# Optimization experiments

Hardware: AMD Instinct MI355X
Metric: run time of the kernel (lower is better)

## Reference

```python
import jax, jax.numpy as jnp
import numpy as np

N_HEAD = 12

def setup_inputs() -> dict:
    key = jax.random.key(0)
    k1, k2, k3 = jax.random.split(key, 3)
    B, T, C = 8, 1024, 768
    x = jax.random.normal(k1, (B, T, C), dtype=jnp.float32)
    # Linear weights stored as [in, out] so y = x @ W + b (same math as torch Linear)
    w_attn = jax.random.normal(k2, (C, 3 * C), dtype=jnp.float32) * (1.0 / np.sqrt(C))
    b_attn = jnp.zeros((3 * C,), dtype=jnp.float32)
    w_proj = jax.random.normal(k3, (C, C), dtype=jnp.float32) * (1.0 / np.sqrt(C))
    b_proj = jnp.zeros((C,), dtype=jnp.float32)
    return {"x": x, "w_attn": w_attn, "b_attn": b_attn, "w_proj": w_proj, "b_proj": b_proj}

def reference(x, w_attn, b_attn, w_proj, b_proj):
    B, T, C = x.shape
    H = N_HEAD
    D = C // H
    qkv = x @ w_attn + b_attn                        # [B,T,3C]
    q, k, v = jnp.split(qkv, 3, axis=-1)             # each [B,T,C]
    q = q.reshape(B, T, H, D).transpose(0, 2, 1, 3)  # [B,H,T,D]
    k = k.reshape(B, T, H, D).transpose(0, 2, 1, 3)
    v = v.reshape(B, T, H, D).transpose(0, 2, 1, 3)
    scale = 1.0 / jnp.sqrt(jnp.asarray(D, dtype=x.dtype))
    att = jnp.einsum('bhqd,bhkd->bhqk', q, k) * scale  # [B,H,T,T]
    causal = jnp.tril(jnp.ones((T, T), dtype=bool))    # [T,T]
    att = jnp.where(causal[None, None], att, jnp.asarray(-jnp.inf, dtype=att.dtype))
    att = jax.nn.softmax(att, axis=-1)
    out = jnp.einsum('bhqk,bhkd->bhqd', att, v)        # [B,H,T,D]
    out = out.transpose(0, 2, 1, 3).reshape(B, T, C)
    return out @ w_proj + b_proj
```

## Files before the change

### kernel.cpp

```cpp
#include <hip/hip_runtime.h>
#include <hip/hip_bf16.h>
#include <cmath>

#define B_ 8
#define T_ 1024
#define C_ 768
#define H_ 12
#define D_ 64
#define N3C 2304
#define M_ 8192

typedef __bf16 bf16x8 __attribute__((ext_vector_type(8)));
typedef float  f32x4  __attribute__((ext_vector_type(4)));

typedef const __attribute__((address_space(1))) void* gptr_t;
typedef __attribute__((address_space(3))) void* lptr_t;

__device__ __forceinline__ bf16x8 cvt_bf16x8(const float4& a, const float4& b) {
    bf16x8 r;
    r[0] = (__bf16)a.x; r[1] = (__bf16)a.y; r[2] = (__bf16)a.z; r[3] = (__bf16)a.w;
    r[4] = (__bf16)b.x; r[5] = (__bf16)b.y; r[6] = (__bf16)b.z; r[7] = (__bf16)b.w;
    return r;
}

__global__ __launch_bounds__(256) void cast_bf16_k(const float* __restrict__ in,
                                                   __bf16* __restrict__ out, int n) {
    int i = (blockIdx.x * 256 + threadIdx.x) * 8;
    if (i >= n) return;
    float4 a = *(const float4*)&in[i];
    float4 b = *(const float4*)&in[i + 4];
    bf16x8 r = cvt_bf16x8(a, b);
    *(bf16x8*)&out[i] = r;
}

__global__ __launch_bounds__(256) void transpose_cast_k(const float* __restrict__ w,
                                                        __bf16* __restrict__ wt,
                                                        int K, int N) {
    __shared__ float tile[32][33];
    int tx = threadIdx.x, ty = threadIdx.y;
    int n0 = blockIdx.x * 32, k0 = blockIdx.y * 32;
#pragma unroll
    for (int i = 0; i < 4; i++)
        tile[ty + i * 8][tx] = w[(size_t)(k0 + ty + i * 8) * N + n0 + tx];
    __syncthreads();
#pragma unroll
    for (int i = 0; i < 4; i++)
        wt[(size_t)(n0 + ty + i * 8) * K + k0 + tx] = (__bf16)tile[tx][ty + i * 8];
}

__global__ __launch_bounds__(256) void qkv_gemm_mfma(const __bf16* __restrict__ A,
                                                     const __bf16* __restrict__ Bt,
                                                     const float* __restrict__ bias,
                                                     __bf16* __restrict__ qb,
                                                     __bf16* __restrict__ kb,
                                                     __bf16* __restrict__ vbt) {
    __shared__ __bf16 smem[128 * 136];
    __bf16* As = smem;
    __bf16* Bs = smem + 128 * 64;
    const int tid = threadIdx.x;
    const int wave = tid >> 6, lane = tid & 63;
    const int lane15 = lane & 15, quad = lane >> 4;
    const int m0 = blockIdx.y * 128, n0 = blockIdx.x * 128;
    const int wm = (wave >> 1) * 64, wn = (wave & 1) * 64;
    f32x4 acc[4][4] = {};

    for (int k0 = 0; k0 < 768; k0 += 64) {
#pragma unroll
        for (int r = 0; r < 4; ++r) {
            int p = r * 256 + tid;
            int mrow = p >> 3, csw = p & 7;
            int ksrc = (csw ^ (mrow & 7)) * 8;
            __builtin_amdgcn_global_load_lds(
                (gptr_t)(A + (size_t)(m0 + mrow) * 768 + k0 + ksrc),
                (lptr_t)(As + (r * 256 + wave * 64) * 8), 16, 0, 0);
            __builtin_amdgcn_global_load_lds(
                (gptr_t)(Bt + (size_t)(n0 + mrow) * 768 + k0 + ksrc),
                (lptr_t)(Bs + (r * 256 + wave * 64) * 8), 16, 0, 0);
        }
        __syncthreads();
#pragma unroll
        for (int ks = 0; ks < 2; ++ks) {
            bf16x8 af[4], bf[4];
#pragma unroll
            for (int mt = 0; mt < 4; ++mt) {
                int m = wm + mt * 16 + lane15;
                int csw = (ks * 4 + quad) ^ (m & 7);
                af[mt] = *(const bf16x8*)(As + m * 64 + csw * 8);
            }
#pragma unroll
            for (int nt = 0; nt < 4; ++nt) {
                int n = wn + nt * 16 + lane15;
                int csw = (ks * 4 + quad) ^ (n & 7);
                bf[nt] = *(const bf16x8*)(Bs + n * 64 + csw * 8);
            }
#pragma unroll
            for (int mt = 0; mt < 4; ++mt)
#pragma unroll
                for (int nt = 0; nt < 4; ++nt)
                    acc[mt][nt] = __builtin_amdgcn_mfma_f32_16x16x32_bf16(af[mt], bf[nt], acc[mt][nt], 0, 0, 0);
        }
        __syncthreads();
    }

    if (n0 < 1536) {
        const bool isq = (n0 < 768);
        const float sc = isq ? 0.125f : 1.0f;
#pragma unroll
        for (int nt = 0; nt < 4; ++nt) {
            int n = n0 + wn + nt * 16 + lane15;
            int rem = isq ? n : (n - 768);
            int h = rem >> 6;
            int d = n & 63;
            float bv = bias[n];
            __bf16* dst = isq ? qb : kb;
#pragma unroll
            for (int mt = 0; mt < 4; ++mt) {
#pragma unroll
                for (int reg = 0; reg < 4; ++reg) {
                    int mrow = m0 + wm + mt * 16 + quad * 4 + reg;
                    int bb = mrow >> 10, t = mrow & 1023;
                    dst[(((size_t)bb * H_ + h) * T_ + t) * D_ + d] =
                        (__bf16)((acc[mt][nt][reg] + bv) * sc);
                }
            }
        }
    } else {
        __bf16* vls = smem;
#pragma unroll
        for (int nt = 0; nt < 4; ++nt) {
            int nl = wn + nt * 16 + lane15;
            float bv = bias[n0 + nl];
#pragma unroll
            for (int mt = 0; mt < 4; ++mt)
#pragma unroll
                for (int reg = 0; reg < 4; ++reg)
                    vls[nl * 136 + wm + mt * 16 + quad * 4 + reg] =
                        (__bf16)(acc[mt][nt][reg] + bv);
        }
        __syncthreads();
        int nl = tid >> 1;
        int t0 = (tid & 1) * 64;
        int n = n0 + nl;
        int h = (n - 1536) >> 6;
        int d = n & 63;
        int bb = m0 >> 10, tg = (m0 & 1023) + t0;
        __bf16* dst = vbt + (((size_t)bb * H_ + h) * D_ + d) * T_ + tg;
        const __bf16* srcl = vls + nl * 136 + t0;
#pragma unroll
        for (int c = 0; c < 8; ++c)
            *(bf16x8*)(dst + c * 8) = *(const bf16x8*)(srcl + c * 8);
    }
}

__global__ __launch_bounds__(256) void proj_gemm_mfma(const __bf16* __restrict__ A,
                                                      const __bf16* __restrict__ Bt,
                                                      const float* __restrict__ bias,
                                                      float* __restrict__ out) {
    __shared__ __bf16 As[128 * 64];
    __shared__ __bf16 Bs[64 * 64];
    const int tid = threadIdx.x;
    const int wave = tid >> 6, lane = tid & 63;
    const int lane15 = lane & 15, quad = lane >> 4;
    const int m0 = blockIdx.y * 128, n0 = blockIdx.x * 64;
    const int wm = wave * 32;
    f32x4 acc[2][4] = {};

    for (int k0 = 0; k0 < 768; k0 += 64) {
#pragma unroll
        for (int r = 0; r < 4; ++r) {
            int p = r * 256 + tid;
            int mrow = p >> 3, csw = p & 7;
            int ksrc = (csw ^ (mrow & 7)) * 8;
            __builtin_amdgcn_global_load_lds(
                (gptr_t)(A + (size_t)(m0 + mrow) * 768 + k0 + ksrc),
                (lptr_t)(As + (r * 256 + wave * 64) * 8), 16, 0, 0);
        }
#pragma unroll
        for (int r = 0; r < 2; ++r) {
            int p = r * 256 + tid;
            int nrow = p >> 3, csw = p & 7;
            int ksrc = (csw ^ (nrow & 7)) * 8;
            __builtin_amdgcn_global_load_lds(
                (gptr_t)(Bt + (size_t)(n0 + nrow) * 768 + k0 + ksrc),
                (lptr_t)(Bs + (r * 256 + wave * 64) * 8), 16, 0, 0);
        }
        __syncthreads();
#pragma unroll
        for (int ks = 0; ks < 2; ++ks) {
            bf16x8 af[2], bf[4];
#pragma unroll
            for (int mt = 0; mt < 2; ++mt) {
                int m = wm + mt * 16 + lane15;
                int csw = (ks * 4 + quad) ^ (m & 7);
                af[mt] = *(const bf16x8*)(As + m * 64 + csw * 8);
            }
#pragma unroll
            for (int nt = 0; nt < 4; ++nt) {
                int n = nt * 16 + lane15;
                int csw = (ks * 4 + quad) ^ (n & 7);
                bf[nt] = *(const bf16x8*)(Bs + n * 64 + csw * 8);
            }
#pragma unroll
            for (int mt = 0; mt < 2; ++mt)
#pragma unroll
                for (int nt = 0; nt < 4; ++nt)
                    acc[mt][nt] = __builtin_amdgcn_mfma_f32_16x16x32_bf16(af[mt], bf[nt], acc[mt][nt], 0, 0, 0);
        }
        __syncthreads();
    }

#pragma unroll
    for (int nt = 0; nt < 4; ++nt) {
        int n = n0 + nt * 16 + lane15;
        float bv = bias[n];
#pragma unroll
        for (int mt = 0; mt < 2; ++mt) {
#pragma unroll
            for (int reg = 0; reg < 4; ++reg) {
                int mrow = m0 + wm + mt * 16 + quad * 4 + reg;
                out[(size_t)mrow * C_ + n] = acc[mt][nt][reg] + bv;
            }
        }
    }
}

__global__ __launch_bounds__(256) void attn_mfma(const __bf16* __restrict__ qb,
                                                 const __bf16* __restrict__ kb,
                                                 const __bf16* __restrict__ vbt,
                                                 __bf16* __restrict__ ao) {
    __shared__ __bf16 Ks[64 * 64];
    __shared__ __bf16 Vts[64 * 64];
    __shared__ __bf16 Ps[4 * 32 * 72];

    const int tid = threadIdx.x;
    const int wave = tid >> 6, lane = tid & 63;
    const int lane15 = lane & 15, quad = lane >> 4;
    const int bh = blockIdx.x;
    const int qt = 7 - blockIdx.y;
    const int b = bh / H_, h = bh % H_;
    const int q0 = qt * 128;

    const __bf16* Kb = kb + (size_t)bh * T_ * D_;
    const __bf16* Vb = vbt + (size_t)bh * D_ * T_;
    __bf16* Pw = Ps + wave * 32 * 72;

    bf16x8 qf[2][2];
#pragma unroll
    for (int g = 0; g < 2; ++g) {
        const __bf16* qrow = qb + ((size_t)bh * T_ + q0 + wave * 32 + g * 16 + lane15) * D_ + quad * 8;
        qf[g][0] = *(const bf16x8*)qrow;
        qf[g][1] = *(const bf16x8*)(qrow + 32);
    }

    f32x4 o[2][4] = {};
    float lsum[2][4] = {};

    const int kunits = 2 * qt + 2;
    for (int ku = 0; ku < kunits; ++ku) {
        const int k0 = ku * 64;
#pragma unroll
        for (int r = 0; r < 2; ++r) {
            int p = r * 256 + tid;
            int row = p >> 3, c = p & 7;
            int cs = (c ^ (row & 7)) * 8;
            __builtin_amdgcn_global_load_lds(
                (gptr_t)(Kb + (size_t)(k0 + row) * D_ + cs),
                (lptr_t)(Ks + (r * 256 + wave * 64) * 8), 16, 0, 0);
            __builtin_amdgcn_global_load_lds(
                (gptr_t)(Vb + (size_t)row * T_ + k0 + cs),
                (lptr_t)(Vts + (r * 256 + wave * 64) * 8), 16, 0, 0);
        }
        __syncthreads();

        f32x4 s[2][4];
#pragma unroll
        for (int kt = 0; kt < 4; ++kt) {
            int row = kt * 16 + lane15;
            bf16x8 kf0 = *(const bf16x8*)(Ks + row * 64 + ((quad) ^ (row & 7)) * 8);
            bf16x8 kf1 = *(const bf16x8*)(Ks + row * 64 + ((4 + quad) ^ (row & 7)) * 8);
#pragma unroll
            for (int g = 0; g < 2; ++g) {
                f32x4 t = {};
                t = __builtin_amdgcn_mfma_f32_16x16x32_bf16(qf[g][0], kf0, t, 0, 0, 0);
                t = __builtin_amdgcn_mfma_f32_16x16x32_bf16(qf[g][1], kf1, t, 0, 0, 0);
                s[g][kt] = t;
            }
        }

        const bool diag = (ku >= 2 * qt);
#pragma unroll
        for (int g = 0; g < 2; ++g) {
#pragma unroll
            for (int kt = 0; kt < 4; ++kt) {
                int col = k0 + kt * 16 + lane15;
#pragma unroll
                for (int r = 0; r < 4; ++r) {
                    float p = __expf(s[g][kt][r]);
                    if (diag) {
                        int qrow = q0 + wave * 32 + g * 16 + quad * 4 + r;
                        if (col > qrow) p = 0.f;
                    }
                    lsum[g][r] += p;
                    Pw[(g * 16 + quad * 4 + r) * 72 + kt * 16 + lane15] = (__bf16)p;
                }
            }
        }

        bf16x8 vf[4][2];
#pragma unroll
        for (int dt = 0; dt < 4; ++dt) {
            int row = dt * 16 + lane15;
#pragma unroll
            for (int half = 0; half < 2; ++half)
                vf[dt][half] = *(const bf16x8*)(Vts + row * 64 + ((half * 4 + quad) ^ (row & 7)) * 8);
        }
#pragma unroll
        for (int g = 0; g < 2; ++g) {
#pragma unroll
            for (int half = 0; half < 2; ++half) {
                bf16x8 pf = *(const bf16x8*)(Pw + (g * 16 + lane15) * 72 + half * 32 + quad * 8);
#pragma unroll
                for (int dt = 0; dt < 4; ++dt)
                    o[g][dt] = __builtin_amdgcn_mfma_f32_16x16x32_bf16(pf, vf[dt][half], o[g][dt], 0, 0, 0);
            }
        }
        __syncthreads();
    }

#pragma unroll
    for (int g = 0; g < 2; ++g) {
        float inv[4];
#pragma unroll
        for (int r = 0; r < 4; ++r) {
            float ls = lsum[g][r];
            ls += __shfl_xor(ls, 1);
            ls += __shfl_xor(ls, 2);
            ls += __shfl_xor(ls, 4);
            ls += __shfl_xor(ls, 8);
            inv[r] = 1.0f / ls;
        }
#pragma unroll
        for (int dt = 0; dt < 4; ++dt) {
#pragma unroll
            for (int r = 0; r < 4; ++r) {
                int t = q0 + wave * 32 + g * 16 + quad * 4 + r;
                ao[((size_t)(b * T_ + t)) * C_ + h * 64 + dt * 16 + lane15] =
                    (__bf16)(o[g][dt][r] * inv[r]);
            }
        }
    }
}

extern "C" void kernel_launch(void* const* d_in, const int* in_sizes, int n_in,
                              void* d_out, int out_size, void* d_ws, size_t ws_size,
                              hipStream_t stream) {
    const float* x = (const float*)d_in[0];
    const float* w_attn = (const float*)d_in[1];
    const float* b_attn = (const float*)d_in[2];
    const float* w_proj = (const float*)d_in[3];
    const float* b_proj = (const float*)d_in[4];
    float* out = (float*)d_out;

    __bf16* xb = (__bf16*)d_ws;
    __bf16* wat = xb + (size_t)M_ * C_;
    __bf16* wpt = wat + (size_t)N3C * C_;
    __bf16* qb = wpt + (size_t)C_ * C_;
    __bf16* kb = qb + (size_t)96 * T_ * D_;
    __bf16* vbt = kb + (size_t)96 * T_ * D_;
    __bf16* ao = vbt + (size_t)96 * T_ * D_;

    cast_bf16_k<<<(M_ * C_) / (256 * 8), 256, 0, stream>>>(x, xb, M_ * C_);
    transpose_cast_k<<<dim3(N3C / 32, C_ / 32), dim3(32, 8), 0, stream>>>(w_attn, wat, C_, N3C);
    transpose_cast_k<<<dim3(C_ / 32, C_ / 32), dim3(32, 8), 0, stream>>>(w_proj, wpt, C_, C_);

    qkv_gemm_mfma<<<dim3(N3C / 128, M_ / 128), 256, 0, stream>>>(xb, wat, b_attn, qb, kb, vbt);
    attn_mfma<<<dim3(96, 8), 256, 0, stream>>>(qb, kb, vbt, ao);
    proj_gemm_mfma<<<dim3(C_ / 64, M_ / 128), 256, 0, stream>>>(ao, wpt, b_proj, out);
}
```

Measured before the change: 199.7 us.

## Double-buffer attention K/V tiles, use exp2 softmax, fuse prepass casts

The attention kernel now double-buffers its K and V tiles in LDS. The next tile's global_load_lds is issued before computing on the current tile, and one barrier per iteration is dropped. Q is pre-scaled by log2(e) in the QKV epilogue so the softmax can use the hardware exp2 instruction instead of __expf. The three prepass kernels (x cast and two weight transpose-casts) are merged into a single launch to cut launch overhead. The cost is doubled LDS for K and V, which may reduce occupancy, and correctness now depends on the earlier barrier protecting the buffer being overwritten.

```diff
diff --git a/kernel.cpp b/kernel.cpp
--- a/kernel.cpp
+++ b/kernel.cpp
@@ -16,6 +16,8 @@
 typedef const __attribute__((address_space(1))) void* gptr_t;
 typedef __attribute__((address_space(3))) void* lptr_t;
 
+#define LOG2E 1.44269504088896f
+
 __device__ __forceinline__ bf16x8 cvt_bf16x8(const float4& a, const float4& b) {
     bf16x8 r;
     r[0] = (__bf16)a.x; r[1] = (__bf16)a.y; r[2] = (__bf16)a.z; r[3] = (__bf16)a.w;
@@ -23,22 +25,34 @@
     return r;
 }
 
-__global__ __launch_bounds__(256) void cast_bf16_k(const float* __restrict__ in,
-                                                   __bf16* __restrict__ out, int n) {
-    int i = (blockIdx.x * 256 + threadIdx.x) * 8;
-    if (i >= n) return;
-    float4 a = *(const float4*)&in[i];
-    float4 b = *(const float4*)&in[i + 4];
-    bf16x8 r = cvt_bf16x8(a, b);
-    *(bf16x8*)&out[i] = r;
-}
-
-__global__ __launch_bounds__(256) void transpose_cast_k(const float* __restrict__ w,
-                                                        __bf16* __restrict__ wt,
-                                                        int K, int N) {
+__global__ __launch_bounds__(256) void prepass(const float* __restrict__ x,
+                                               __bf16* __restrict__ xb,
+                                               const float* __restrict__ wa,
+                                               __bf16* __restrict__ wat,
+                                               const float* __restrict__ wp,
+                                               __bf16* __restrict__ wpt) {
     __shared__ float tile[32][33];
-    int tx = threadIdx.x, ty = threadIdx.y;
-    int n0 = blockIdx.x * 32, k0 = blockIdx.y * 32;
+    const int bx = blockIdx.x, tid = threadIdx.x;
+    if (bx < 3072) {
+        int i = (bx * 256 + tid) * 8;
+        float4 a = *(const float4*)&x[i];
+        float4 b = *(const float4*)&x[i + 4];
+        *(bf16x8*)&xb[i] = cvt_bf16x8(a, b);
+        return;
+    }
+    const float* w;
+    __bf16* wt;
+    int K, N, n0, k0;
+    if (bx < 4800) {
+        int bb = bx - 3072;
+        w = wa; wt = wat; K = 768; N = 2304;
+        n0 = (bb % 72) * 32; k0 = (bb / 72) * 32;
+    } else {
+        int bb = bx - 4800;
+        w = wp; wt = wpt; K = 768; N = 768;
+        n0 = (bb % 24) * 32; k0 = (bb / 24) * 32;
+    }
+    int tx = tid & 31, ty = tid >> 5;
 #pragma unroll
     for (int i = 0; i < 4; i++)
         tile[ty + i * 8][tx] = w[(size_t)(k0 + ty + i * 8) * N + n0 + tx];
@@ -104,7 +118,7 @@
 
     if (n0 < 1536) {
         const bool isq = (n0 < 768);
-        const float sc = isq ? 0.125f : 1.0f;
+        const float sc = isq ? (0.125f * LOG2E) : 1.0f;
 #pragma unroll
         for (int nt = 0; nt < 4; ++nt) {
             int n = n0 + wn + nt * 16 + lane15;
@@ -228,8 +242,8 @@
                                                  const __bf16* __restrict__ kb,
                                                  const __bf16* __restrict__ vbt,
                                                  __bf16* __restrict__ ao) {
-    __shared__ __bf16 Ks[64 * 64];
-    __shared__ __bf16 Vts[64 * 64];
+    __shared__ __bf16 Ks[2][64 * 64];
+    __shared__ __bf16 Vts[2][64 * 64];
     __shared__ __bf16 Ps[4 * 32 * 72];
 
     const int tid = threadIdx.x;
@@ -256,28 +270,39 @@
     float lsum[2][4] = {};
 
     const int kunits = 2 * qt + 2;
+
+#define STAGE(KU, BUF)                                                             \
+    {                                                                              \
+        const int k0s = (KU) * 64;                                                 \
+        _Pragma("unroll")                                                          \
+        for (int r = 0; r < 2; ++r) {                                              \
+            int p = r * 256 + tid;                                                 \
+            int row = p >> 3, c = p & 7;                                           \
+            int cs = (c ^ (row & 7)) * 8;                                          \
+            __builtin_amdgcn_global_load_lds(                                      \
+                (gptr_t)(Kb + (size_t)(k0s + row) * D_ + cs),                      \
+                (lptr_t)(&Ks[BUF][0] + (r * 256 + wave * 64) * 8), 16, 0, 0);      \
+            __builtin_amdgcn_global_load_lds(                                      \
+                (gptr_t)(Vb + (size_t)row * T_ + k0s + cs),                        \
+                (lptr_t)(&Vts[BUF][0] + (r * 256 + wave * 64) * 8), 16, 0, 0);     \
+        }                                                                          \
+    }
+
+    STAGE(0, 0);
+
     for (int ku = 0; ku < kunits; ++ku) {
+        __syncthreads();
+        if (ku + 1 < kunits) STAGE(ku + 1, (ku + 1) & 1);
+        const __bf16* Kc = &Ks[ku & 1][0];
+        const __bf16* Vc = &Vts[ku & 1][0];
         const int k0 = ku * 64;
-#pragma unroll
-        for (int r = 0; r < 2; ++r) {
-            int p = r * 256 + tid;
-            int row = p >> 3, c = p & 7;
-            int cs = (c ^ (row & 7)) * 8;
-            __builtin_amdgcn_global_load_lds(
-                (gptr_t)(Kb + (size_t)(k0 + row) * D_ + cs),
-                (lptr_t)(Ks + (r * 256 + wave * 64) * 8), 16, 0, 0);
-            __builtin_amdgcn_global_load_lds(
-                (gptr_t)(Vb + (size_t)row * T_ + k0 + cs),
-                (lptr_t)(Vts + (r * 256 + wave * 64) * 8), 16, 0, 0);
-        }
-        __syncthreads();
 
         f32x4 s[2][4];
 #pragma unroll
         for (int kt = 0; kt < 4; ++kt) {
             int row = kt * 16 + lane15;
-            bf16x8 kf0 = *(const bf16x8*)(Ks + row * 64 + ((quad) ^ (row & 7)) * 8);
-            bf16x8 kf1 = *(const bf16x8*)(Ks + row * 64 + ((4 + quad) ^ (row & 7)) * 8);
+            bf16x8 kf0 = *(const bf16x8*)(Kc + row * 64 + ((quad) ^ (row & 7)) * 8);
+            bf16x8 kf1 = *(const bf16x8*)(Kc + row * 64 + ((4 + quad) ^ (row & 7)) * 8);
 #pragma unroll
             for (int g = 0; g < 2; ++g) {
                 f32x4 t = {};
@@ -295,7 +320,7 @@
                 int col = k0 + kt * 16 + lane15;
 #pragma unroll
                 for (int r = 0; r < 4; ++r) {
-                    float p = __expf(s[g][kt][r]);
+                    float p = __builtin_amdgcn_exp2f(s[g][kt][r]);
                     if (diag) {
                         int qrow = q0 + wave * 32 + g * 16 + quad * 4 + r;
                         if (col > qrow) p = 0.f;
@@ -312,7 +337,7 @@
             int row = dt * 16 + lane15;
 #pragma unroll
             for (int half = 0; half < 2; ++half)
-                vf[dt][half] = *(const bf16x8*)(Vts + row * 64 + ((half * 4 + quad) ^ (row & 7)) * 8);
+                vf[dt][half] = *(const bf16x8*)(Vc + row * 64 + ((half * 4 + quad) ^ (row & 7)) * 8);
         }
 #pragma unroll
         for (int g = 0; g < 2; ++g) {
@@ -324,7 +349,6 @@
                     o[g][dt] = __builtin_amdgcn_mfma_f32_16x16x32_bf16(pf, vf[dt][half], o[g][dt], 0, 0, 0);
             }
         }
-        __syncthreads();
     }
 
 #pragma unroll
@@ -369,10 +393,7 @@
     __bf16* vbt = kb + (size_t)96 * T_ * D_;
     __bf16* ao = vbt + (size_t)96 * T_ * D_;
 
-    cast_bf16_k<<<(M_ * C_) / (256 * 8), 256, 0, stream>>>(x, xb, M_ * C_);
-    transpose_cast_k<<<dim3(N3C / 32, C_ / 32), dim3(32, 8), 0, stream>>>(w_attn, wat, C_, N3C);
-    transpose_cast_k<<<dim3(C_ / 32, C_ / 32), dim3(32, 8), 0, stream>>>(w_proj, wpt, C_, C_);
-
+    prepass<<<5376, 256, 0, stream>>>(x, xb, w_attn, wat, w_proj, wpt);
     qkv_gemm_mfma<<<dim3(N3C / 128, M_ / 128), 256, 0, stream>>>(xb, wat, b_attn, qb, kb, vbt);
     attn_mfma<<<dim3(96, 8), 256, 0, stream>>>(qb, kb, vbt, ao);
     proj_gemm_mfma<<<dim3(C_ / 64, M_ / 128), 256, 0, stream>>>(ao, wpt, b_proj, out);
```

New measurement: 194.8 us. 2.4% less time.
